# Optimization experiments

Hardware: AMD Instinct MI355X
Metric: run time of the kernel (lower is better)

The kernel has to match this reference:

```python
import jax, jax.numpy as jnp
import numpy as np

N_HEAD = 8
EPS = 1e-6  # LayerNorm2d eps


def setup_inputs() -> dict:
    key = jax.random.key(0)
    ks = jax.random.split(key, 7)
    B, C, H, W = 16, 256, 128, 128
    nh, dk, dv = N_HEAD, 32, 32
    s = 1.0 / np.sqrt(C)
    return {
        "q": jax.random.normal(ks[0], (B, C, H, W), jnp.float32),
        "k": jax.random.normal(ks[1], (B, C, H, W), jnp.float32),
        "v": jax.random.normal(ks[2], (B, C, H, W), jnp.float32),
        # 1x1 convs without bias == channel matmuls; weight shape [out_ch, in_ch]
        "wq": jax.random.normal(ks[3], (nh * dk, C), jnp.float32) * s,
        "wk": jax.random.normal(ks[4], (nh * dk, C), jnp.float32) * s,
        "wv": jax.random.normal(ks[5], (nh * dv, C), jnp.float32) * s,
        "wfc": jax.random.normal(ks[6], (C, nh * dv), jnp.float32) * (1.0 / np.sqrt(nh * dv)),
        "ln_w": jnp.ones((C,), jnp.float32),
        "ln_b": jnp.zeros((C,), jnp.float32),
        "kernel": 5,
        "pad": 2,
    }


def _forward(q, k, v, wq, wk, wv, wfc, ln_w, ln_b, kernel, pad):
    B, C, H, W = q.shape
    nh = N_HEAD
    dk = wq.shape[0] // nh
    dv = wv.shape[0] // nh
    assert kernel == 2 * pad + 1
    residual = q
    # 1x1 conv projections, split into heads: [B, nh, d, H, W]
    qh = jnp.einsum('oc,bchw->bohw', wq, q).reshape(B, nh, dk, H, W)
    kh = jnp.einsum('oc,bchw->bohw', wk, k).reshape(B, nh, dk, H, W)
    vh = jnp.einsum('oc,bchw->bohw', wv, v).reshape(B, nh, dv, H, W)
    # zero-pad spatially: out-of-bounds correlations/values are zero, matching the
    # original bilinear sampler (zeros padding) and the custom padding() helper.
    kp = jnp.pad(kh, ((0, 0), (0, 0), (0, 0), (pad, pad), (pad, pad)))
    vp = jnp.pad(vh, ((0, 0), (0, 0), (0, 0), (pad, pad), (pad, pad)))
    # local correlation volume: dot(q[i,j], k[i+dy-pad, j+dx-pad]) for the KxK window
    # (integer offsets -> bilinear sample degenerates to a gather). Never materializes
    # the full [B, HW, HW] matrix the torch code builds before sampling.
    corr = jnp.stack(
        [jnp.einsum('bncij,bncij->bnij', qh, kp[:, :, :, dy:dy + H, dx:dx + W])
         for dy in range(kernel) for dx in range(kernel)], axis=-1)  # [B,nh,H,W,K*K]
    # relu (from CorrBlock.corr), temperature = sqrt(d_k), softmax over window.
    # OOB entries are 0 (not -inf), faithfully matching the original.
    attn = jax.nn.softmax(jax.nn.relu(corr) / jnp.float32(np.sqrt(dk)), axis=-1)
    # channel attention: per-pixel weighted sum of v over the same window
    out = jnp.zeros((B, nh, dv, H, W), q.dtype)
    idx = 0
    for dy in range(kernel):
        for dx in range(kernel):
            out = out + attn[:, :, :, :, idx][:, :, None] * vp[:, :, :, dy:dy + H, dx:dx + W]
            idx += 1
    o = jnp.einsum('oc,bchw->bohw', wfc, out.reshape(B, nh * dv, H, W)) + residual
    # LayerNorm2d: normalize over channel dim per pixel
    mu = o.mean(1, keepdims=True)
    var = ((o - mu) ** 2).mean(1, keepdims=True)
    y = (o - mu) / jnp.sqrt(var + EPS)
    return ln_w[None, :, None, None] * y + ln_b[None, :, None, None]


def reference(q, k, v, wq, wk, wv, wfc, ln_w, ln_b, kernel, pad):
    return _forward(q, k, v, wq, wk, wv, wfc, ln_w, ln_b, kernel, pad)
```

## Files before the change

kernel.cpp:

```cpp
#include <hip/hip_runtime.h>
#include <hip/hip_bf16.h>

#define BATCH 16
#define CH 256
#define HH 128
#define WW 128
#define HWSZ (HH * WW)
#define NHEAD 8
#define DHEAD 32
#define PW 132
#define PPIX (132 * 132)
#define LDSTB 40

typedef __attribute__((ext_vector_type(8))) short bf16x8;
typedef __attribute__((ext_vector_type(4))) float f32x4;
typedef _Float16 h2v __attribute__((ext_vector_type(2)));

__device__ __forceinline__ unsigned short f2b(float f) {
    unsigned u = __builtin_bit_cast(unsigned, f);
    u += 0x7fffu + ((u >> 16) & 1u);
    return (unsigned short)(u >> 16);
}
__device__ __forceinline__ unsigned short f2h(float f) {
    _Float16 h = (_Float16)f;
    return __builtin_bit_cast(unsigned short, h);
}
__device__ __forceinline__ unsigned pkbf(float a, float b) {
    __hip_bfloat162_raw r = __hip_bfloat162_raw(__float22bfloat162_rn(make_float2(a, b)));
    return (unsigned)r.x | ((unsigned)r.y << 16);
}

#if __has_builtin(__builtin_amdgcn_fdot2)
#define DOT2(a, b, c) __builtin_amdgcn_fdot2((a), (b), (c), false)
#else
#define DOT2(a, b, c) ((c) + (float)(a)[0] * (float)(b)[0] + (float)(a)[1] * (float)(b)[1])
#endif

__global__ __launch_bounds__(256)
void zpad_kernel(unsigned short* __restrict__ kpad, unsigned short* __restrict__ vpad)
{
    int bid = blockIdx.x;
    unsigned short* dst = ((bid & 1) ? vpad : kpad) + (size_t)(bid >> 1) * PPIX * DHEAD;
    const uint4 z = {0u, 0u, 0u, 0u};
    for (int i = threadIdx.x; i < 1040; i += 256) {
        int row, col;
        if (i < 264)      { row = i / 132; col = i - row * 132; }
        else if (i < 528) { int j = i - 264; int r = j / 132; row = 130 + r; col = j - r * 132; }
        else              { int j = i - 528; row = 2 + (j >> 2); int c = j & 3; col = (c < 2) ? c : (128 + c); }
        uint4* p = reinterpret_cast<uint4*>(dst + (size_t)(row * PW + col) * DHEAD);
        p[0] = z; p[1] = z; p[2] = z; p[3] = z;
    }
}

__global__ __launch_bounds__(256)
void prep_kernel(const float* __restrict__ wq, const float* __restrict__ wk,
                 const float* __restrict__ wv, const float* __restrict__ wfc,
                 unsigned short* __restrict__ wb)
{
    const float* src = (blockIdx.y == 0) ? wq : (blockIdx.y == 1) ? wk
                     : (blockIdx.y == 2) ? wv : wfc;
    unsigned short* dst = wb + blockIdx.y * 65536;
    int e = (blockIdx.x * 256 + threadIdx.x) * 8;
    const float4* s = reinterpret_cast<const float4*>(src + e);
    float4 a = s[0], c = s[1];
    uint4 u;
    u.x = pkbf(a.x, a.y); u.y = pkbf(a.z, a.w);
    u.z = pkbf(c.x, c.y); u.w = pkbf(c.z, c.w);
    *reinterpret_cast<uint4*>(dst + e) = u;
}

__global__ __launch_bounds__(256)
void proj_kernel(const float* __restrict__ q, const float* __restrict__ k,
                 const float* __restrict__ v, const unsigned short* __restrict__ wb,
                 unsigned short* __restrict__ qh, unsigned short* __restrict__ kpad,
                 unsigned short* __restrict__ vpad)
{
    __shared__ __align__(16) unsigned short lB[2][64 * LDSTB];

    const int t = threadIdx.x;
    const int b = blockIdx.y;
    const int p0 = blockIdx.x * 64;
    const int z = blockIdx.z;

    const float* X; unsigned short* Y;
    if (z == 0)      { X = q; Y = qh; }
    else if (z == 1) { X = k; Y = kpad; }
    else             { X = v; Y = vpad; }
    const unsigned short* Wb = wb + z * 65536;
    X += (size_t)b * CH * HWSZ;
    const size_t pixstride = (z == 0) ? (size_t)HWSZ : (size_t)PPIX;
    Y += (size_t)b * NHEAD * pixstride * DHEAD;

    const int lane = t & 63;
    const int wid  = t >> 6;
    const int lrow = lane & 15;
    const int lkg  = lane >> 4;
    const int pB   = t & 63;
    const int cg   = t >> 6;

    float fv[8];
    {
        const float* xp = X + (size_t)(cg * 8) * HWSZ + p0 + pB;
#pragma unroll
        for (int i = 0; i < 8; ++i) fv[i] = xp[(size_t)i * HWSZ];
    }
    bf16x8 afc[4], afn[4];
#pragma unroll
    for (int m = 0; m < 4; ++m)
        afc[m] = *reinterpret_cast<const bf16x8*>(Wb + (wid * 64 + m * 16 + lrow) * 256 + lkg * 8);

    f32x4 acc[4][4];
    const f32x4 zero = {0.f, 0.f, 0.f, 0.f};
#pragma unroll
    for (int m = 0; m < 4; ++m)
#pragma unroll
        for (int n = 0; n < 4; ++n) acc[m][n] = zero;

    for (int ks = 0; ks < 8; ++ks) {
        {
            uint4 u;
            u.x = pkbf(fv[0], fv[1]); u.y = pkbf(fv[2], fv[3]);
            u.z = pkbf(fv[4], fv[5]); u.w = pkbf(fv[6], fv[7]);
            *reinterpret_cast<uint4*>(&lB[ks & 1][pB * LDSTB + cg * 8]) = u;
        }
        if (ks < 7) {
            const float* xp = X + (size_t)((ks + 1) * 32 + cg * 8) * HWSZ + p0 + pB;
#pragma unroll
            for (int i = 0; i < 8; ++i) fv[i] = xp[(size_t)i * HWSZ];
        }
        __syncthreads();
        if (ks < 7) {
#pragma unroll
            for (int m = 0; m < 4; ++m)
                afn[m] = *reinterpret_cast<const bf16x8*>(Wb + (wid * 64 + m * 16 + lrow) * 256 + (ks + 1) * 32 + lkg * 8);
        }
        bf16x8 bfv[4];
#pragma unroll
        for (int n = 0; n < 4; ++n)
            bfv[n] = *reinterpret_cast<const bf16x8*>(&lB[ks & 1][(n * 16 + lrow) * LDSTB + lkg * 8]);
#pragma unroll
        for (int m = 0; m < 4; ++m)
#pragma unroll
            for (int n = 0; n < 4; ++n)
                acc[m][n] = __builtin_amdgcn_mfma_f32_16x16x32_bf16(afc[m], bfv[n], acc[m][n], 0, 0, 0);
#pragma unroll
        for (int m = 0; m < 4; ++m) afc[m] = afn[m];
    }

    const int lr = lane >> 4, lc = lane & 15;
#pragma unroll
    for (int m = 0; m < 4; ++m)
#pragma unroll
        for (int n = 0; n < 4; ++n) {
            int o = wid * 64 + m * 16 + lr * 4;
            int hh_ = o >> 5, d0 = o & 31;
            int p = p0 + n * 16 + lc;
            ushort4 pk;
            pk.x = f2h(acc[m][n][0]); pk.y = f2h(acc[m][n][1]);
            pk.z = f2h(acc[m][n][2]); pk.w = f2h(acc[m][n][3]);
            size_t pix;
            if (z == 0) pix = (size_t)hh_ * HWSZ + p;
            else { int row = p >> 7, col = p & 127; pix = (size_t)hh_ * PPIX + (size_t)(row + 2) * PW + (col + 2); }
            *reinterpret_cast<ushort4*>(&Y[pix * DHEAD + d0]) = pk;
        }
}

__global__ __launch_bounds__(1024)
void attn_kernel(unsigned short* __restrict__ qh,
                 const unsigned short* __restrict__ kpad,
                 const unsigned short* __restrict__ vpad)
{
    const int t = threadIdx.x;
    const int swz = (blockIdx.x & 7) * 1024 + (blockIdx.x >> 3);
    const int bh = swz >> 6;
    const int tile = swz & 63;
    const int x0 = (tile & 7) * 16, y0 = (tile >> 3) * 16;
    const int qc = t & 3;
    const int px = (t >> 2) & 15;
    const int py = t >> 6;
    const int gx = x0 + px, gy = y0 + py;

    unsigned short* qp = qh + ((size_t)bh * HWSZ + gy * WW + gx) * DHEAD + qc * 8;
    const unsigned short* kb = kpad + (size_t)bh * PPIX * DHEAD + qc * 8;
    const unsigned short* vb = vpad + (size_t)bh * PPIX * DHEAD + qc * 8;

    union { uint4 u; h2v h2[4]; } Q;
    Q.u = *reinterpret_cast<const uint4*>(qp);

    float ew[25];
#pragma unroll
    for (int wy = 0; wy < 5; ++wy) {
        const unsigned short* krow = kb + (size_t)((gy + wy) * PW + gx) * DHEAD;
#pragma unroll
        for (int wx = 0; wx < 5; ++wx) {
            union { uint4 u; h2v h2[4]; } K;
            K.u = *reinterpret_cast<const uint4*>(krow + wx * DHEAD);
            float s = 0.f;
#pragma unroll
            for (int j = 0; j < 4; ++j)
                s = DOT2(Q.h2[j], K.h2[j], s);
            s += __shfl_xor(s, 1);
            s += __shfl_xor(s, 2);
            ew[wy * 5 + wx] = __expf(fmaxf(s, 0.f) * 0.17677669529663687f);
        }
    }

    float sum = 0.f;
#pragma unroll
    for (int i = 0; i < 25; ++i) sum += ew[i];
    const float inv = 1.f / sum;

    union { uint4 u; h2v h2[4]; } A;
    const h2v hz = {(_Float16)0.f, (_Float16)0.f};
#pragma unroll
    for (int j = 0; j < 4; ++j) A.h2[j] = hz;

#pragma unroll
    for (int wy = 0; wy < 5; ++wy) {
        const unsigned short* vrow = vb + (size_t)((gy + wy) * PW + gx) * DHEAD;
#pragma unroll
        for (int wx = 0; wx < 5; ++wx) {
            _Float16 wh = (_Float16)(ew[wy * 5 + wx] * inv);
            h2v w2 = {wh, wh};
            union { uint4 u; h2v h2[4]; } V;
            V.u = *reinterpret_cast<const uint4*>(vrow + wx * DHEAD);
#pragma unroll
            for (int j = 0; j < 4; ++j)
                A.h2[j] += w2 * V.h2[j];
        }
    }

    uint4 o;
    o.x = pkbf((float)A.h2[0][0], (float)A.h2[0][1]);
    o.y = pkbf((float)A.h2[1][0], (float)A.h2[1][1]);
    o.z = pkbf((float)A.h2[2][0], (float)A.h2[2][1]);
    o.w = pkbf((float)A.h2[3][0], (float)A.h2[3][1]);
    *reinterpret_cast<uint4*>(qp) = o;
}

__global__ __launch_bounds__(256)
void fcln_kernel(const unsigned short* __restrict__ ob, const unsigned short* __restrict__ wfcb,
                 const float* __restrict__ qres, const float* __restrict__ lnw,
                 const float* __restrict__ lnb, float* __restrict__ out)
{
    __shared__ __align__(16) unsigned short lB[2][64 * LDSTB];
    __shared__ float lsum[4][64];
    __shared__ float lssq[4][64];

    const int t = threadIdx.x;
    const int b = blockIdx.y;
    const int p0 = blockIdx.x * 64;

    const int lane = t & 63;
    const int wid  = t >> 6;
    const int lrow = lane & 15;
    const int lkg  = lane >> 4;
    const int pxs  = t >> 2;
    const int qcs  = t & 3;

    uint4 bv;
    {
        const unsigned short* obb = ob + (size_t)(b * NHEAD + 0) * HWSZ * DHEAD;
        bv = *reinterpret_cast<const uint4*>(obb + (size_t)(p0 + pxs) * DHEAD + qcs * 8);
    }
    bf16x8 afc[4], afn[4];
#pragma unroll
    for (int m = 0; m < 4; ++m)
        afc[m] = *reinterpret_cast<const bf16x8*>(wfcb + (wid * 64 + m * 16 + lrow) * 256 + lkg * 8);

    f32x4 acc[4][4];
    const f32x4 zero = {0.f, 0.f, 0.f, 0.f};
#pragma unroll
    for (int m = 0; m < 4; ++m)
#pragma unroll
        for (int n = 0; n < 4; ++n) acc[m][n] = zero;

    for (int ks = 0; ks < 8; ++ks) {
        *reinterpret_cast<uint4*>(&lB[ks & 1][pxs * LDSTB + qcs * 8]) = bv;
        if (ks < 7) {
            const unsigned short* obb = ob + (size_t)(b * NHEAD + ks + 1) * HWSZ * DHEAD;
            bv = *reinterpret_cast<const uint4*>(obb + (size_t)(p0 + pxs) * DHEAD + qcs * 8);
        }
        __syncthreads();
        if (ks < 7) {
#pragma unroll
            for (int m = 0; m < 4; ++m)
                afn[m] = *reinterpret_cast<const bf16x8*>(wfcb + (wid * 64 + m * 16 + lrow) * 256 + (ks + 1) * 32 + lkg * 8);
        }
        bf16x8 bfv[4];
#pragma unroll
        for (int n = 0; n < 4; ++n)
            bfv[n] = *reinterpret_cast<const bf16x8*>(&lB[ks & 1][(n * 16 + lrow) * LDSTB + lkg * 8]);
#pragma unroll
        for (int m = 0; m < 4; ++m)
#pragma unroll
            for (int n = 0; n < 4; ++n)
                acc[m][n] = __builtin_amdgcn_mfma_f32_16x16x32_bf16(afc[m], bfv[n], acc[m][n], 0, 0, 0);
#pragma unroll
        for (int m = 0; m < 4; ++m) afc[m] = afn[m];
    }

    const int lr = lane >> 4, lc = lane & 15;
    const float* qb = qres + (size_t)b * CH * HWSZ;
#pragma unroll
    for (int m = 0; m < 4; ++m)
#pragma unroll
        for (int n = 0; n < 4; ++n)
#pragma unroll
            for (int j = 0; j < 4; ++j) {
                int o = wid * 64 + m * 16 + lr * 4 + j;
                int p = p0 + n * 16 + lc;
                acc[m][n][j] += qb[(size_t)o * HWSZ + p];
            }

    float s[4], s2[4];
#pragma unroll
    for (int n = 0; n < 4; ++n) {
        float a = 0.f, c2 = 0.f;
#pragma unroll
        for (int m = 0; m < 4; ++m)
#pragma unroll
            for (int j = 0; j < 4; ++j) {
                float x = acc[m][n][j];
                a += x; c2 += x * x;
            }
        a  += __shfl_xor(a, 16);  a  += __shfl_xor(a, 32);
        c2 += __shfl_xor(c2, 16); c2 += __shfl_xor(c2, 32);
        s[n] = a; s2[n] = c2;
    }
    if (lane < 16) {
#pragma unroll
        for (int n = 0; n < 4; ++n) {
            lsum[wid][n * 16 + lane] = s[n];
            lssq[wid][n * 16 + lane] = s2[n];
        }
    }
    __syncthreads();

    float mu[4], rs[4];
#pragma unroll
    for (int n = 0; n < 4; ++n) {
        int p = n * 16 + lc;
        float ts = lsum[0][p] + lsum[1][p] + lsum[2][p] + lsum[3][p];
        float tq = lssq[0][p] + lssq[1][p] + lssq[2][p] + lssq[3][p];
        float m_ = ts * (1.f / 256.f);
        float v_ = tq * (1.f / 256.f) - m_ * m_;
        mu[n] = m_;
        rs[n] = rsqrtf(v_ + 1e-6f);
    }

    float* op = out + (size_t)b * CH * HWSZ;
#pragma unroll
    for (int m = 0; m < 4; ++m)
#pragma unroll
        for (int j = 0; j < 4; ++j) {
            int o = wid * 64 + m * 16 + lr * 4 + j;
            float g = lnw[o], bb = lnb[o];
#pragma unroll
            for (int n = 0; n < 4; ++n) {
                int p = p0 + n * 16 + lc;
                op[(size_t)o * HWSZ + p] = (acc[m][n][j] - mu[n]) * rs[n] * g + bb;
            }
        }
}

extern "C" void kernel_launch(void* const* d_in, const int* in_sizes, int n_in,
                              void* d_out, int out_size, void* d_ws, size_t ws_size,
                              hipStream_t stream) {
    const float* q   = (const float*)d_in[0];
    const float* k   = (const float*)d_in[1];
    const float* v   = (const float*)d_in[2];
    const float* wq  = (const float*)d_in[3];
    const float* wk  = (const float*)d_in[4];
    const float* wv  = (const float*)d_in[5];
    const float* wfc = (const float*)d_in[6];
    const float* lnw = (const float*)d_in[7];
    const float* lnb = (const float*)d_in[8];

    const size_t qsz = (size_t)BATCH * NHEAD * HWSZ * DHEAD;
    const size_t psz = (size_t)BATCH * NHEAD * PPIX * DHEAD;
    if (ws_size < (qsz + 2 * psz + 4 * 65536) * sizeof(unsigned short)) return;

    unsigned short* qh = (unsigned short*)d_ws;
    unsigned short* kp = qh + qsz;
    unsigned short* vp = kp + psz;
    unsigned short* wb = vp + psz;

    zpad_kernel<<<256, 256, 0, stream>>>(kp, vp);
    prep_kernel<<<dim3(32, 4), 256, 0, stream>>>(wq, wk, wv, wfc, wb);
    proj_kernel<<<dim3(HWSZ / 64, BATCH, 3), 256, 0, stream>>>(q, k, v, wb, qh, kp, vp);
    attn_kernel<<<8192, 1024, 0, stream>>>(qh, kp, vp);
    fcln_kernel<<<dim3(HWSZ / 64, BATCH), 256, 0, stream>>>(qh, wb + 3 * 65536, q, lnw, lnb, (float*)d_out);
}
```

Before: 798.5 us.

## Stage full K slab in LDS once instead of double-buffered per-step staging

```diff
diff --git a/kernel.cpp b/kernel.cpp
--- a/kernel.cpp
+++ b/kernel.cpp
@@ -10,17 +10,12 @@
 #define DHEAD 32
 #define PW 132
 #define PPIX (132 * 132)
-#define LDSTB 40
+#define ROWS 264
 
 typedef __attribute__((ext_vector_type(8))) short bf16x8;
 typedef __attribute__((ext_vector_type(4))) float f32x4;
 typedef _Float16 h2v __attribute__((ext_vector_type(2)));
 
-__device__ __forceinline__ unsigned short f2b(float f) {
-    unsigned u = __builtin_bit_cast(unsigned, f);
-    u += 0x7fffu + ((u >> 16) & 1u);
-    return (unsigned short)(u >> 16);
-}
 __device__ __forceinline__ unsigned short f2h(float f) {
     _Float16 h = (_Float16)f;
     return __builtin_bit_cast(unsigned short, h);
@@ -75,7 +70,7 @@
                  unsigned short* __restrict__ qh, unsigned short* __restrict__ kpad,
                  unsigned short* __restrict__ vpad)
 {
-    __shared__ __align__(16) unsigned short lB[2][64 * LDSTB];
+    __shared__ __align__(16) unsigned short lB[64 * ROWS];
 
     const int t = threadIdx.x;
     const int b = blockIdx.y;
@@ -98,12 +93,18 @@
     const int pB   = t & 63;
     const int cg   = t >> 6;
 
-    float fv[8];
-    {
-        const float* xp = X + (size_t)(cg * 8) * HWSZ + p0 + pB;
-#pragma unroll
-        for (int i = 0; i < 8; ++i) fv[i] = xp[(size_t)i * HWSZ];
-    }
+#pragma unroll
+    for (int i = 0; i < 8; ++i) {
+        const float* xp = X + (size_t)((cg * 8 + i) * 8) * HWSZ + p0 + pB;
+        float fv[8];
+#pragma unroll
+        for (int j = 0; j < 8; ++j) fv[j] = xp[(size_t)j * HWSZ];
+        uint4 u;
+        u.x = pkbf(fv[0], fv[1]); u.y = pkbf(fv[2], fv[3]);
+        u.z = pkbf(fv[4], fv[5]); u.w = pkbf(fv[6], fv[7]);
+        *reinterpret_cast<uint4*>(&lB[pB * ROWS + (cg * 8 + i) * 8]) = u;
+    }
+
     bf16x8 afc[4], afn[4];
 #pragma unroll
     for (int m = 0; m < 4; ++m)
@@ -116,19 +117,10 @@
 #pragma unroll
         for (int n = 0; n < 4; ++n) acc[m][n] = zero;
 
+    __syncthreads();
+
+#pragma unroll
     for (int ks = 0; ks < 8; ++ks) {
-        {
-            uint4 u;
-            u.x = pkbf(fv[0], fv[1]); u.y = pkbf(fv[2], fv[3]);
-            u.z = pkbf(fv[4], fv[5]); u.w = pkbf(fv[6], fv[7]);
-            *reinterpret_cast<uint4*>(&lB[ks & 1][pB * LDSTB + cg * 8]) = u;
-        }
-        if (ks < 7) {
-            const float* xp = X + (size_t)((ks + 1) * 32 + cg * 8) * HWSZ + p0 + pB;
-#pragma unroll
-            for (int i = 0; i < 8; ++i) fv[i] = xp[(size_t)i * HWSZ];
-        }
-        __syncthreads();
         if (ks < 7) {
 #pragma unroll
             for (int m = 0; m < 4; ++m)
@@ -137,7 +129,7 @@
         bf16x8 bfv[4];
 #pragma unroll
         for (int n = 0; n < 4; ++n)
-            bfv[n] = *reinterpret_cast<const bf16x8*>(&lB[ks & 1][(n * 16 + lrow) * LDSTB + lkg * 8]);
+            bfv[n] = *reinterpret_cast<const bf16x8*>(&lB[(n * 16 + lrow) * ROWS + (ks * 4 + lkg) * 8]);
 #pragma unroll
         for (int m = 0; m < 4; ++m)
 #pragma unroll
@@ -243,7 +235,7 @@
                  const float* __restrict__ qres, const float* __restrict__ lnw,
                  const float* __restrict__ lnb, float* __restrict__ out)
 {
-    __shared__ __align__(16) unsigned short lB[2][64 * LDSTB];
+    __shared__ __align__(16) unsigned short lB[64 * ROWS];
     __shared__ float lsum[4][64];
     __shared__ float lssq[4][64];
 
@@ -255,14 +247,16 @@
     const int wid  = t >> 6;
     const int lrow = lane & 15;
     const int lkg  = lane >> 4;
-    const int pxs  = t >> 2;
-    const int qcs  = t & 3;
-
-    uint4 bv;
-    {
-        const unsigned short* obb = ob + (size_t)(b * NHEAD + 0) * HWSZ * DHEAD;
-        bv = *reinterpret_cast<const uint4*>(obb + (size_t)(p0 + pxs) * DHEAD + qcs * 8);
-    }
+    const int pxf  = t >> 2;
+    const int qcf  = t & 3;
+
+#pragma unroll
+    for (int h = 0; h < 8; ++h) {
+        uint4 bv = *reinterpret_cast<const uint4*>(
+            ob + ((size_t)(b * NHEAD + h) * HWSZ + p0 + pxf) * DHEAD + qcf * 8);
+        *reinterpret_cast<uint4*>(&lB[pxf * ROWS + (h * 4 + qcf) * 8]) = bv;
+    }
+
     bf16x8 afc[4], afn[4];
 #pragma unroll
     for (int m = 0; m < 4; ++m)
@@ -275,13 +269,10 @@
 #pragma unroll
         for (int n = 0; n < 4; ++n) acc[m][n] = zero;
 
+    __syncthreads();
+
+#pragma unroll
     for (int ks = 0; ks < 8; ++ks) {
-        *reinterpret_cast<uint4*>(&lB[ks & 1][pxs * LDSTB + qcs * 8]) = bv;
-        if (ks < 7) {
-            const unsigned short* obb = ob + (size_t)(b * NHEAD + ks + 1) * HWSZ * DHEAD;
-            bv = *reinterpret_cast<const uint4*>(obb + (size_t)(p0 + pxs) * DHEAD + qcs * 8);
-        }
-        __syncthreads();
         if (ks < 7) {
 #pragma unroll
             for (int m = 0; m < 4; ++m)
@@ -290,7 +281,7 @@
         bf16x8 bfv[4];
 #pragma unroll
         for (int n = 0; n < 4; ++n)
-            bfv[n] = *reinterpret_cast<const bf16x8*>(&lB[ks & 1][(n * 16 + lrow) * LDSTB + lkg * 8]);
+            bfv[n] = *reinterpret_cast<const bf16x8*>(&lB[(n * 16 + lrow) * ROWS + (ks * 4 + lkg) * 8]);
 #pragma unroll
         for (int m = 0; m < 4; ++m)
 #pragma unroll
```

Result: faster. 776.5 us (-2.8%).
